# Kernel tuning notes

Measured on AMD Instinct MI355X. Metric: run time of the kernel, lower is better.

The kernel has to match this reference:

```python
import jax, jax.numpy as jnp
import numpy as np

N, E = 50000, 300000
IN, FC, AC, H, C1, C2, OUT = 1024, 128, 20, 4, 10, 5, 3
FCN = FC + AC + H * C2  # 168


def bn_eval(x, g, b):
    # BatchNorm1d in eval mode with running_mean=0, running_var=1
    return x * (g / jnp.sqrt(1.0 + 1e-5)) + b


def add_self_loops(edge_index, edge_attr, n):
    # PyG add_self_loops with fill_value='mean': self-loop attr = mean of incoming edge attrs
    src, dst = edge_index[0], edge_index[1]
    ones = jnp.ones(src.shape[0], jnp.float32)
    deg = jax.ops.segment_sum(ones, dst, num_segments=n)
    mean_attr = jax.ops.segment_sum(edge_attr, dst, num_segments=n) / jnp.maximum(deg, 1.0)[:, None]
    loop = jnp.arange(n, dtype=src.dtype)
    return (jnp.concatenate([src, loop]), jnp.concatenate([dst, loop]),
            jnp.concatenate([edge_attr, mean_attr], 0))


def gatv2(x, src, dst, eattr, Wl, bl, Wr, br, We, att, b, n):
    # GATv2Conv (concat=True, negative_slope=0.2, edge_dim=1)
    h, c = att.shape
    xl = (x @ Wl + bl).reshape(n, h, c)
    xr = (x @ Wr + br).reshape(n, h, c)
    em = (eattr @ We).reshape(-1, h, c)
    m = jax.nn.leaky_relu(xl[src] + xr[dst] + em, 0.2)   # [E', H, C]
    logit = jnp.einsum('ehc,hc->eh', m, att)              # [E', H]
    mx = jax.ops.segment_max(logit, dst, num_segments=n)
    ex = jnp.exp(logit - mx[dst])
    den = jax.ops.segment_sum(ex, dst, num_segments=n)
    alpha = ex / (den[dst] + 1e-16)                       # segment softmax over dst
    out = jax.ops.segment_sum(xl[src] * alpha[..., None], dst, num_segments=n)
    return out.reshape(n, h * c) + b


def setup_inputs() -> dict:
    key = jax.random.key(0)
    ks = jax.random.split(key, 24)
    rn = lambda k, s: jax.random.normal(k, s, jnp.float32) * 0.05
    return {
        'features': jax.random.normal(ks[0], (N, IN), jnp.float32),
        'edges': jax.random.randint(ks[1], (2, E), 0, N),
        'edges2': jax.random.randint(ks[2], (2, E), 0, N),
        'edge_features': jax.random.normal(ks[3], (E, 1), jnp.float32),
        'additional_features': jax.random.normal(ks[4], (N, AC), jnp.float32),
        'sage_Wl': rn(ks[5], (IN, FC)), 'sage_bl': jnp.zeros((FC,), jnp.float32),
        'sage_Wr': rn(ks[6], (IN, FC)),
        'g1_Wl': rn(ks[7], (AC, H * C1)), 'g1_bl': jnp.zeros((H * C1,), jnp.float32),
        'g1_Wr': rn(ks[8], (AC, H * C1)), 'g1_br': jnp.zeros((H * C1,), jnp.float32),
        'g1_We': rn(ks[9], (1, H * C1)), 'g1_att': rn(ks[10], (H, C1)),
        'g1_b': jnp.zeros((H * C1,), jnp.float32),
        'g2_Wl': rn(ks[11], (H * C1, H * C2)), 'g2_bl': jnp.zeros((H * C2,), jnp.float32),
        'g2_Wr': rn(ks[12], (H * C1, H * C2)), 'g2_br': jnp.zeros((H * C2,), jnp.float32),
        'g2_We': rn(ks[13], (1, H * C2)), 'g2_att': rn(ks[14], (H, C2)),
        'g2_b': jnp.zeros((H * C2,), jnp.float32),
        'fc1_W': rn(ks[15], (FCN, FCN)), 'fc1_b': jnp.zeros((FCN,), jnp.float32),
        'fc2_W': rn(ks[16], (FCN, OUT)), 'fc2_b': jnp.zeros((OUT,), jnp.float32),
        'bnx_g': jnp.ones((FC,), jnp.float32), 'bnx_b': jnp.zeros((FC,), jnp.float32),
        'bny_g': jnp.ones((H * C2,), jnp.float32), 'bny_b': jnp.zeros((H * C2,), jnp.float32),
        'bnf_g': jnp.ones((FCN,), jnp.float32), 'bnf_b': jnp.zeros((FCN,), jnp.float32),
    }


def reference(features, edges, edges2, edge_features, additional_features,
              sage_Wl, sage_bl, sage_Wr,
              g1_Wl, g1_bl, g1_Wr, g1_br, g1_We, g1_att, g1_b,
              g2_Wl, g2_bl, g2_Wr, g2_br, g2_We, g2_att, g2_b,
              fc1_W, fc1_b, fc2_W, fc2_b,
              bnx_g, bnx_b, bny_g, bny_b, bnf_g, bnf_b):
    n = features.shape[0]
    # --- SAGEConv (mean aggr): out = lin_l(mean_j x_j) + lin_r(x_i) ---
    src, dst = edges[0], edges[1]
    deg = jax.ops.segment_sum(jnp.ones(src.shape[0], jnp.float32), dst, num_segments=n)
    aggr = jax.ops.segment_sum(features[src], dst, num_segments=n) / jnp.maximum(deg, 1.0)[:, None]
    x = aggr @ sage_Wl + sage_bl + features @ sage_Wr
    x = bn_eval(x, bnx_g, bnx_b)
    # --- GATv2 stack (self loops with mean edge-attr fill) ---
    s2, d2, ea = add_self_loops(edges2, edge_features, n)
    y = gatv2(additional_features, s2, d2, ea, g1_Wl, g1_bl, g1_Wr, g1_br, g1_We, g1_att, g1_b, n)
    y = jax.nn.leaky_relu(y, 0.01)  # activation (dropout off in eval)
    y = gatv2(y, s2, d2, ea, g2_Wl, g2_bl, g2_Wr, g2_br, g2_We, g2_att, g2_b, n)
    y = bn_eval(y, bny_g, bny_b)
    # --- MLP head ---
    z = jax.nn.leaky_relu(jnp.concatenate([x, y], axis=1), 0.01)
    z = jnp.concatenate([z, additional_features], axis=1) @ fc1_W + fc1_b
    z = jax.nn.relu(bn_eval(z, bnf_g, bnf_b))
    return z @ fc2_W + fc2_b
```

## Files before the change

kernel.cpp:

```cpp
#include <hip/hip_runtime.h>
#include <hip/hip_bf16.h>
#include <cfloat>

__device__ __forceinline__ float lrelu(float x, float a) { return x > 0.0f ? x : a * x; }

__device__ __forceinline__ unsigned short f2bf(float f) {
    unsigned u = __float_as_uint(f);
    unsigned r = (u + 0x7FFFu + ((u >> 16) & 1u)) >> 16;
    return (unsigned short)r;
}
__device__ __forceinline__ float bf2f(unsigned short u) {
    return __uint_as_float((unsigned)u << 16);
}

typedef __attribute__((ext_vector_type(8))) short short8;
typedef __attribute__((ext_vector_type(4))) float f32x4;

#define BN_RSQ 0.99999500003749968750f
#define SCAN_B 256

__global__ void zero_ws(uint4* __restrict__ p, int n16)
{
    int t = blockIdx.x * blockDim.x + threadIdx.x;
    if (t < n16) p[t] = make_uint4(0u, 0u, 0u, 0u);
}

__global__ void prep_all(const float* __restrict__ sWl, const float* __restrict__ sWr,
                         unsigned short* __restrict__ Btp,
                         const float* __restrict__ fc1W, unsigned short* __restrict__ Bt1p,
                         const float* __restrict__ g1Wl, const float* __restrict__ g1Wr,
                         unsigned short* __restrict__ Bg1,
                         const float* __restrict__ g2Wl, const float* __restrict__ g2Wr,
                         unsigned short* __restrict__ Bg2,
                         const int* __restrict__ e1d, const int* __restrict__ e2d,
                         const float* __restrict__ ef,
                         int* __restrict__ cnt1, int* __restrict__ cnt2,
                         float* __restrict__ easum, float* __restrict__ eaext, int E)
{
    int idx = blockIdx.x * blockDim.x + threadIdx.x;
    if (idx < 262144) {
        int j = idx & 7, lane = (idx >> 3) & 63, fn = (idx >> 9) & 3, wid = (idx >> 11) & 3, t = idx >> 13;
        int c = wid * 64 + fn * 16 + (lane & 15);
        int k = t * 32 + (lane >> 4) * 8 + j;
        float v = (c < 128) ? sWl[(size_t)k * 128 + c] : sWr[(size_t)k * 128 + (c - 128)];
        Btp[idx] = f2bf(v);
        return;
    }
    idx -= 262144;
    if (idx < 36864) {
        int j = idx & 7, lane = (idx >> 3) & 63, fn = (idx >> 9) & 3, q = idx >> 11;
        int wid = q % 3, t = q / 3;
        int c = wid * 64 + fn * 16 + (lane & 15);
        int k = t * 32 + (lane >> 4) * 8 + j;
        float v = (c < 168 && k < 168) ? fc1W[(size_t)k * 168 + c] : 0.0f;
        Bt1p[idx] = f2bf(v);
        return;
    }
    idx -= 36864;
    if (idx < 2560) {
        int j = idx & 7, lane = (idx >> 3) & 63, fn = idx >> 9;
        int c = fn * 16 + (lane & 15);
        int k = (lane >> 4) * 8 + j;
        float v = 0.0f;
        if (k < 20) v = (c < 40) ? g1Wl[(size_t)k * 40 + c] : g1Wr[(size_t)k * 40 + (c - 40)];
        Bg1[idx] = f2bf(v);
        return;
    }
    idx -= 2560;
    if (idx < 3072) {
        int j = idx & 7, lane = (idx >> 3) & 63, q = idx >> 9;
        int fn = q % 3, t = q / 3;
        int c = fn * 16 + (lane & 15);
        int k = t * 32 + (lane >> 4) * 8 + j;
        float v = 0.0f;
        if (k < 40 && c < 40) v = (c < 20) ? g2Wl[(size_t)k * 20 + c] : g2Wr[(size_t)k * 20 + (c - 20)];
        Bg2[idx] = f2bf(v);
        return;
    }
    idx -= 3072;
    if (idx < E) {
        atomicAdd(&cnt1[e1d[idx]], 1);
        int d2 = e2d[idx];
        atomicAdd(&cnt2[d2], 1);
        float a = ef[idx];
        atomicAdd(&easum[d2], a);
        eaext[idx] = a;
    }
}

__global__ __launch_bounds__(256) void gemm_sage_mfma(
    const float* __restrict__ A, const unsigned short* __restrict__ Btp,
    unsigned short* __restrict__ P, int M)
{
    __shared__ unsigned short As2[2][64][72];
    const int tid = threadIdx.x;
    const int wid = tid >> 6, lane = tid & 63;
    const int m0 = blockIdx.x * 64;
    const int l16 = lane & 15, g = lane >> 4;
    const int colbase = wid * 64 + l16;
    const short8* Bv = reinterpret_cast<const short8*>(Btp);
    const int srow = tid >> 4, scol = (tid & 15) * 4;

    f32x4 acc[4][4] = {};
    float4 rcur[4], rnext[4];

#pragma unroll
    for (int p = 0; p < 4; ++p) {
        int ar = m0 + p * 16 + srow;
        rcur[p] = make_float4(0.f, 0.f, 0.f, 0.f);
        if (ar < M) rcur[p] = *reinterpret_cast<const float4*>(&A[(size_t)ar * 1024 + scol]);
    }
#pragma unroll
    for (int p = 0; p < 4; ++p) {
        ushort4 u;
        u.x = f2bf(rcur[p].x); u.y = f2bf(rcur[p].y); u.z = f2bf(rcur[p].z); u.w = f2bf(rcur[p].w);
        *reinterpret_cast<ushort4*>(&As2[0][p * 16 + srow][scol]) = u;
    }
#pragma unroll
    for (int p = 0; p < 4; ++p) {
        int ar = m0 + p * 16 + srow;
        rcur[p] = make_float4(0.f, 0.f, 0.f, 0.f);
        if (ar < M) rcur[p] = *reinterpret_cast<const float4*>(&A[(size_t)ar * 1024 + 64 + scol]);
    }
    __syncthreads();

    for (int c = 0; c < 16; ++c) {
        const int buf = c & 1;
        if (c < 14) {
            const int k0 = (c + 2) * 64;
#pragma unroll
            for (int p = 0; p < 4; ++p) {
                int ar = m0 + p * 16 + srow;
                rnext[p] = make_float4(0.f, 0.f, 0.f, 0.f);
                if (ar < M) rnext[p] = *reinterpret_cast<const float4*>(&A[(size_t)ar * 1024 + k0 + scol]);
            }
        }
#pragma unroll
        for (int t = 0; t < 2; ++t) {
            const int ks = c * 2 + t;
            short8 afr[4], bfr[4];
#pragma unroll
            for (int fm = 0; fm < 4; ++fm)
                afr[fm] = *reinterpret_cast<const short8*>(&As2[buf][fm * 16 + l16][t * 32 + g * 8]);
#pragma unroll
            for (int fn = 0; fn < 4; ++fn)
                bfr[fn] = Bv[((ks * 4 + wid) * 4 + fn) * 64 + lane];
#pragma unroll
            for (int fm = 0; fm < 4; ++fm)
#pragma unroll
                for (int fn = 0; fn < 4; ++fn)
                    acc[fm][fn] = __builtin_amdgcn_mfma_f32_16x16x32_bf16(
                        afr[fm], bfr[t == 0 ? fn : fn], acc[fm][fn], 0, 0, 0);
        }
        if (c < 15) {
#pragma unroll
            for (int p = 0; p < 4; ++p) {
                ushort4 u;
                u.x = f2bf(rcur[p].x); u.y = f2bf(rcur[p].y);
                u.z = f2bf(rcur[p].z); u.w = f2bf(rcur[p].w);
                *reinterpret_cast<ushort4*>(&As2[buf ^ 1][p * 16 + srow][scol]) = u;
            }
        }
        __syncthreads();
#pragma unroll
        for (int p = 0; p < 4; ++p) rcur[p] = rnext[p];
    }

#pragma unroll
    for (int fm = 0; fm < 4; ++fm) {
#pragma unroll
        for (int r = 0; r < 4; ++r) {
            int row = m0 + fm * 16 + g * 4 + r;
            if (row < M) {
#pragma unroll
                for (int fn = 0; fn < 4; ++fn)
                    P[(size_t)row * 256 + colbase + fn * 16] = f2bf(acc[fm][fn][r]);
            }
        }
    }
}

template <int IND, int KS, int NF, int MODE>
__global__ __launch_bounds__(64) void gat_lin_mfma(
    const float* __restrict__ X, const unsigned short* __restrict__ Bp,
    const float* __restrict__ bl, const float* __restrict__ br,
    float* __restrict__ xl, float* __restrict__ xr, int M)
{
    constexpr int W = KS * 32;
    constexpr int WP = W + 8;
    __shared__ unsigned short xs[64][WP];
    const int lane = threadIdx.x;
    const int m0 = blockIdx.x * 64;
    const int l16 = lane & 15, g = lane >> 4;
    const short8* Bv = reinterpret_cast<const short8*>(Bp);

    constexpr int NV = 64 * IND / 4 / 64;
#pragma unroll
    for (int i = 0; i < NV; ++i) {
        int q = i * 64 + lane;
        int f = q * 4;
        int row = f / IND, col = f % IND;
        int ar = m0 + row;
        float4 v = make_float4(0.f, 0.f, 0.f, 0.f);
        if (ar < M) v = *reinterpret_cast<const float4*>(&X[(size_t)ar * IND + col]);
        ushort4 u;
        u.x = f2bf(v.x); u.y = f2bf(v.y); u.z = f2bf(v.z); u.w = f2bf(v.w);
        *reinterpret_cast<ushort4*>(&xs[row][col]) = u;
    }
    ushort4 zz; zz.x = 0; zz.y = 0; zz.z = 0; zz.w = 0;
#pragma unroll
    for (int c = IND; c < W; c += 4)
        *reinterpret_cast<ushort4*>(&xs[lane][c]) = zz;

    f32x4 acc[4][NF] = {};
#pragma unroll
    for (int t = 0; t < KS; ++t) {
        short8 afr[4], bfr[NF];
#pragma unroll
        for (int fm = 0; fm < 4; ++fm)
            afr[fm] = *reinterpret_cast<const short8*>(&xs[fm * 16 + l16][t * 32 + g * 8]);
#pragma unroll
        for (int fn = 0; fn < NF; ++fn)
            bfr[fn] = Bv[(t * NF + fn) * 64 + lane];
#pragma unroll
        for (int fm = 0; fm < 4; ++fm)
#pragma unroll
            for (int fn = 0; fn < NF; ++fn)
                acc[fm][fn] = __builtin_amdgcn_mfma_f32_16x16x32_bf16(
                    afr[fm], bfr[fn], acc[fm][fn], 0, 0, 0);
    }

#pragma unroll
    for (int fm = 0; fm < 4; ++fm) {
#pragma unroll
        for (int r = 0; r < 4; ++r) {
            int row = m0 + fm * 16 + g * 4 + r;
            if (row < M) {
#pragma unroll
                for (int fn = 0; fn < NF; ++fn) {
                    int col = fn * 16 + l16;
                    float v = acc[fm][fn][r];
                    if (MODE == 1) {
                        if (col < 40) xl[(size_t)row * 40 + col] = v + bl[col];
                        else          xr[(size_t)row * 40 + (col - 40)] = v + br[col - 40];
                    } else {
                        if (col < 20)      xl[(size_t)row * 20 + col] = v + bl[col];
                        else if (col < 40) xr[(size_t)row * 20 + (col - 20)] = v + br[col - 20];
                    }
                }
            }
        }
    }
}

__global__ __launch_bounds__(256) void mlp_mfma(
    const unsigned short* __restrict__ z, const float* __restrict__ addf,
    const unsigned short* __restrict__ Bt1p,
    const float* __restrict__ fc1b, const float* __restrict__ bnfg, const float* __restrict__ bnfb,
    const float* __restrict__ fc2W, const float* __restrict__ fc2b,
    float* __restrict__ out, int M)
{
    __shared__ __align__(16) char smem[64 * 169 * 4];
    unsigned short (*zs)[200] = reinterpret_cast<unsigned short(*)[200]>(smem);
    float (*ts)[169] = reinterpret_cast<float(*)[169]>(smem);
    const int tid = threadIdx.x;
    const int wid = tid >> 6, lane = tid & 63;
    const int m0 = blockIdx.x * 64;
    const int l16 = lane & 15, g = lane >> 4;
    const short8* Bv = reinterpret_cast<const short8*>(Bt1p);

#pragma unroll
    for (int p = 0; p < 13; ++p) {
        int idx = p * 256 + tid;
        if (idx < 3200) {
            int row = idx / 50, c4 = (idx % 50) * 4;
            int ar = m0 + row;
            ushort4 u; u.x = 0; u.y = 0; u.z = 0; u.w = 0;
            if (ar < M) {
                if (c4 < 148) {
                    u = *reinterpret_cast<const ushort4*>(&z[(size_t)ar * 168 + c4]);
                } else if (c4 < 168) {
                    float4 v = *reinterpret_cast<const float4*>(&addf[(size_t)ar * 20 + (c4 - 148)]);
                    u.x = f2bf(v.x); u.y = f2bf(v.y); u.z = f2bf(v.z); u.w = f2bf(v.w);
                }
            }
            *reinterpret_cast<ushort4*>(&zs[row][c4]) = u;
        }
    }
    __syncthreads();

    f32x4 acc[4][4] = {};
    if (wid < 3) {
#pragma unroll
        for (int t = 0; t < 6; ++t) {
            short8 afr[4], bfr[4];
#pragma unroll
            for (int fm = 0; fm < 4; ++fm)
                afr[fm] = *reinterpret_cast<const short8*>(&zs[fm * 16 + l16][t * 32 + g * 8]);
#pragma unroll
            for (int fn = 0; fn < 4; ++fn)
                bfr[fn] = Bv[((t * 3 + wid) * 4 + fn) * 64 + lane];
#pragma unroll
            for (int fm = 0; fm < 4; ++fm)
#pragma unroll
                for (int fn = 0; fn < 4; ++fn)
                    acc[fm][fn] = __builtin_amdgcn_mfma_f32_16x16x32_bf16(
                        afr[fm], bfr[fn], acc[fm][fn], 0, 0, 0);
        }
    }
    __syncthreads();
    if (wid < 3) {
        const int colbase = wid * 64 + l16;
#pragma unroll
        for (int fm = 0; fm < 4; ++fm) {
#pragma unroll
            for (int r = 0; r < 4; ++r) {
                int rr = fm * 16 + g * 4 + r;
#pragma unroll
                for (int fn = 0; fn < 4; ++fn) {
                    int col = colbase + fn * 16;
                    if (col < 168) {
                        float v = acc[fm][fn][r] + fc1b[col];
                        v = v * (bnfg[col] * BN_RSQ) + bnfb[col];
                        ts[rr][col] = fmaxf(v, 0.0f);
                    }
                }
            }
        }
    }
    __syncthreads();
    if (tid < 192) {
        int r = tid & 63, c = tid >> 6;
        float acc2 = fc2b[c];
#pragma unroll 4
        for (int k = 0; k < 168; ++k) acc2 += ts[r][k] * fc2W[k * 3 + c];
        int row = m0 + r;
        if (row < M) out[(size_t)row * 3 + c] = acc2;
    }
}

__global__ void scan1(const int* __restrict__ cnt1, const int* __restrict__ cnt2,
                      int* __restrict__ off1, int* __restrict__ off2,
                      int* __restrict__ bsum1, int* __restrict__ bsum2, int M)
{
    __shared__ int sh[SCAN_B];
    int y = blockIdx.y;
    const int* cnt = y ? cnt2 : cnt1;
    int* excl = y ? off2 : off1;
    int* bsum = y ? bsum2 : bsum1;
    int i = blockIdx.x * SCAN_B + threadIdx.x;
    int v = (i < M) ? cnt[i] + y : 0;
    sh[threadIdx.x] = v;
    __syncthreads();
    for (int o = 1; o < SCAN_B; o <<= 1) {
        int t = (threadIdx.x >= o) ? sh[threadIdx.x - o] : 0;
        __syncthreads();
        sh[threadIdx.x] += t;
        __syncthreads();
    }
    if (i < M) excl[i] = sh[threadIdx.x] - v;
    if (threadIdx.x == SCAN_B - 1) bsum[blockIdx.x] = sh[threadIdx.x];
}

__global__ void scan2(int* __restrict__ bsum1, int* __restrict__ bsum2, int nb)
{
    __shared__ int sh[SCAN_B];
    int* bsum = blockIdx.y ? bsum2 : bsum1;
    int v = ((int)threadIdx.x < nb) ? bsum[threadIdx.x] : 0;
    sh[threadIdx.x] = v;
    __syncthreads();
    for (int o = 1; o < SCAN_B; o <<= 1) {
        int t = (threadIdx.x >= o) ? sh[threadIdx.x - o] : 0;
        __syncthreads();
        sh[threadIdx.x] += t;
        __syncthreads();
    }
    if ((int)threadIdx.x < nb) bsum[threadIdx.x] = sh[threadIdx.x] - v;
}

__global__ void scan3(int* __restrict__ off1, int* __restrict__ off2,
                      const int* __restrict__ bsum1, const int* __restrict__ bsum2,
                      const int* __restrict__ cnt1, const int* __restrict__ cnt2,
                      const float* __restrict__ easum, float* __restrict__ eaext,
                      int E, int M)
{
    int y = blockIdx.y;
    int* off = y ? off2 : off1;
    const int* bsum = y ? bsum2 : bsum1;
    const int* cnt = y ? cnt2 : cnt1;
    int i = blockIdx.x * SCAN_B + threadIdx.x;
    if (i < M) {
        int v = off[i] + bsum[blockIdx.x];
        off[i] = v;
        if (i == M - 1) off[M] = v + cnt[i] + y;
        if (y) eaext[E + i] = easum[i] / fmaxf((float)cnt2[i], 1.0f);
    }
}

__global__ void fill_both(const int* __restrict__ e1s, const int* __restrict__ e1d,
                          const int* __restrict__ e2d,
                          const int* __restrict__ off1, const int* __restrict__ off2,
                          int* __restrict__ cnt1, int* __restrict__ cnt2,
                          int* __restrict__ srcs1, int* __restrict__ eidx2, int E, int Eext)
{
    int t = blockIdx.x * blockDim.x + threadIdx.x;
    if (t < E) {
        int d = e1d[t];
        int pos = atomicSub(&cnt1[d], 1) - 1;
        srcs1[off1[d] + pos] = e1s[t];
    }
    int t2 = t - E;
    if (t2 >= 0 && t2 < Eext) {
        if (t2 < E) {
            int d = e2d[t2];
            int pos = atomicSub(&cnt2[d], 1) - 1;
            eidx2[off2[d] + pos] = t2;
        } else {
            int nn = t2 - E;
            eidx2[off2[nn + 1] - 1] = t2;
        }
    }
}

__global__ void sage_gather(const int* __restrict__ srcs1, const int* __restrict__ off1,
                            const unsigned short* __restrict__ P, const float* __restrict__ bl,
                            const float* __restrict__ bng, const float* __restrict__ bnb,
                            unsigned short* __restrict__ z, int N)
{
    int t = blockIdx.x * blockDim.x + threadIdx.x;
    if (t >= N * 32) return;
    int n = t >> 5, g = t & 31;
    int beg = off1[n], end = off1[n + 1];
    float a0 = 0.f, a1 = 0.f, a2 = 0.f, a3 = 0.f;
    for (int j = beg; j < end; ++j) {
        int s = srcs1[j];
        ushort4 v = *reinterpret_cast<const ushort4*>(&P[(size_t)s * 256 + g * 4]);
        a0 += bf2f(v.x); a1 += bf2f(v.y); a2 += bf2f(v.z); a3 += bf2f(v.w);
    }
    float inv = 1.0f / fmaxf((float)(end - beg), 1.0f);
    ushort4 pr = *reinterpret_cast<const ushort4*>(&P[(size_t)n * 256 + 128 + g * 4]);
    float a4[4] = {a0, a1, a2, a3};
    float p4[4] = {bf2f(pr.x), bf2f(pr.y), bf2f(pr.z), bf2f(pr.w)};
    ushort4 zo;
    unsigned short* zp = reinterpret_cast<unsigned short*>(&zo);
#pragma unroll
    for (int k = 0; k < 4; ++k) {
        int cc = g * 4 + k;
        float x = a4[k] * inv + bl[cc] + p4[k];
        x = x * (bng[cc] * BN_RSQ) + bnb[cc];
        zp[k] = f2bf(lrelu(x, 0.01f));
    }
    *reinterpret_cast<ushort4*>(&z[(size_t)n * 168 + g * 4]) = zo;
}

template <int H, int C, int MODE>
__global__ void gat_node(const int* __restrict__ eidx2, const int* __restrict__ off2,
                         const int* __restrict__ e2s, const float* __restrict__ eaext,
                         const float* __restrict__ xl, const float* __restrict__ xr,
                         const float* __restrict__ We, const float* __restrict__ att,
                         const float* __restrict__ b,
                         const float* __restrict__ bng, const float* __restrict__ bnb,
                         void* __restrict__ outv, int E, int N)
{
    int t = blockIdx.x * blockDim.x + threadIdx.x;
    if (t >= N * H) return;
    int n = t / H, h = t % H;

    float xrc[C], atth[C], weh[C];
#pragma unroll
    for (int c = 0; c < C; ++c) {
        xrc[c]  = xr[(size_t)n * (H * C) + h * C + c];
        atth[c] = att[h * C + c];
        weh[c]  = We[h * C + c];
    }

    const int beg = off2[n], end = off2[n + 1];

    float mx = -FLT_MAX, den = 0.0f;
    float accv[C] = {};
    for (int j = beg; j < end; ++j) {
        int e = eidx2[j];
        int s = (e < E) ? e2s[e] : (e - E);
        float ea = eaext[e];
        const float* xls = xl + (size_t)s * (H * C) + h * C;
        float xv[C];
        float lg = 0.0f;
#pragma unroll
        for (int c = 0; c < C; ++c) {
            xv[c] = xls[c];
            float m = xv[c] + xrc[c] + ea * weh[c];
            lg += lrelu(m, 0.2f) * atth[c];
        }
        if (lg > mx) {
            float sc = __expf(mx - lg);
            den *= sc;
#pragma unroll
            for (int c = 0; c < C; ++c) accv[c] *= sc;
            mx = lg;
        }
        float ex = __expf(lg - mx);
        den += ex;
#pragma unroll
        for (int c = 0; c < C; ++c) accv[c] += ex * xv[c];
    }
    float inv = 1.0f / (den + 1e-16f);

#pragma unroll
    for (int c = 0; c < C; ++c) {
        int jch = h * C + c;
        float v = accv[c] * inv + b[jch];
        if (MODE == 1) {
            ((float*)outv)[(size_t)n * (H * C) + jch] = lrelu(v, 0.01f);
        } else {
            v = v * (bng[jch] * BN_RSQ) + bnb[jch];
            ((unsigned short*)outv)[(size_t)n * 168 + 128 + jch] = f2bf(lrelu(v, 0.01f));
        }
    }
}

extern "C" void kernel_launch(void* const* d_in, const int* in_sizes, int n_in,
                              void* d_out, int out_size, void* d_ws, size_t ws_size,
                              hipStream_t stream)
{
    const float* features = (const float*)d_in[0];
    const int*   e1       = (const int*)d_in[1];
    const int*   e2       = (const int*)d_in[2];
    const float* ef       = (const float*)d_in[3];
    const float* addf     = (const float*)d_in[4];
    const float* sage_Wl  = (const float*)d_in[5];
    const float* sage_bl  = (const float*)d_in[6];
    const float* sage_Wr  = (const float*)d_in[7];
    const float* g1_Wl = (const float*)d_in[8];
    const float* g1_bl = (const float*)d_in[9];
    const float* g1_Wr = (const float*)d_in[10];
    const float* g1_br = (const float*)d_in[11];
    const float* g1_We = (const float*)d_in[12];
    const float* g1_att = (const float*)d_in[13];
    const float* g1_b = (const float*)d_in[14];
    const float* g2_Wl = (const float*)d_in[15];
    const float* g2_bl = (const float*)d_in[16];
    const float* g2_Wr = (const float*)d_in[17];
    const float* g2_br = (const float*)d_in[18];
    const float* g2_We = (const float*)d_in[19];
    const float* g2_att = (const float*)d_in[20];
    const float* g2_b = (const float*)d_in[21];
    const float* fc1_W = (const float*)d_in[22];
    const float* fc1_b = (const float*)d_in[23];
    const float* fc2_W = (const float*)d_in[24];
    const float* fc2_b = (const float*)d_in[25];
    const float* bnx_g = (const float*)d_in[26];
    const float* bnx_b = (const float*)d_in[27];
    const float* bny_g = (const float*)d_in[28];
    const float* bny_b = (const float*)d_in[29];
    const float* bnf_g = (const float*)d_in[30];
    const float* bnf_b = (const float*)d_in[31];

    const int N = in_sizes[0] / 1024;
    const int E = in_sizes[3];
    const int Eext = E + N;
    const int* e1s = e1, *e1d = e1 + E;
    const int* e2s = e2, *e2d = e2 + E;
    const int nb = (N + SCAN_B - 1) / SCAN_B;

    char* wb = (char*)d_ws;
    size_t off = 0;
    auto takeB = [&](size_t bytes) { char* p = wb + off; off = (off + bytes + 255) & ~(size_t)255; return p; };
    unsigned short* P = (unsigned short*)takeB((size_t)N * 256 * 2);
    unsigned short* z = (unsigned short*)takeB((size_t)N * 168 * 2);
    float* eaext = (float*)takeB((size_t)Eext * 4);
    float* xl1   = (float*)takeB((size_t)N * 40 * 4);
    float* xr1   = (float*)takeB((size_t)N * 40 * 4);
    float* y1    = (float*)takeB((size_t)N * 40 * 4);
    float* xl2   = (float*)takeB((size_t)N * 20 * 4);
    float* xr2   = (float*)takeB((size_t)N * 20 * 4);
    unsigned short* Btp  = (unsigned short*)takeB((size_t)256 * 1024 * 2);
    unsigned short* Bt1p = (unsigned short*)takeB((size_t)36864 * 2);
    unsigned short* Bg1  = (unsigned short*)takeB((size_t)2560 * 2);
    unsigned short* Bg2  = (unsigned short*)takeB((size_t)3072 * 2);
    char* zero_beg = wb + off;
    int* cnt1    = (int*)takeB((size_t)N * 4);
    int* cnt2    = (int*)takeB((size_t)N * 4);
    float* easum = (float*)takeB((size_t)N * 4);
    size_t zero_len = (size_t)((wb + off) - zero_beg);
    int* off1  = (int*)takeB((size_t)(N + 1) * 4);
    int* off2  = (int*)takeB((size_t)(N + 1) * 4);
    int* bsum1 = (int*)takeB(SCAN_B * 4);
    int* bsum2 = (int*)takeB(SCAN_B * 4);
    int* srcs1 = (int*)takeB((size_t)E * 4);
    int* eidx2 = (int*)takeB((size_t)Eext * 4);

    const int B = 256;
    const int n16 = (int)(zero_len / 16);
    zero_ws<<<(n16 + B - 1) / B, B, 0, stream>>>((uint4*)zero_beg, n16);

    const int prep_total = 262144 + 36864 + 2560 + 3072 + E;
    prep_all<<<(prep_total + B - 1) / B, B, 0, stream>>>(
        sage_Wl, sage_Wr, Btp, fc1_W, Bt1p,
        g1_Wl, g1_Wr, Bg1, g2_Wl, g2_Wr, Bg2,
        e1d, e2d, ef, cnt1, cnt2, easum, eaext, E);

    scan1<<<dim3(nb, 2), SCAN_B, 0, stream>>>(cnt1, cnt2, off1, off2, bsum1, bsum2, N);
    scan2<<<dim3(1, 2), SCAN_B, 0, stream>>>(bsum1, bsum2, nb);
    scan3<<<dim3(nb, 2), SCAN_B, 0, stream>>>(off1, off2, bsum1, bsum2, cnt1, cnt2,
                                              easum, eaext, E, N);

    fill_both<<<(E + Eext + B - 1) / B, B, 0, stream>>>(e1s, e1d, e2d, off1, off2,
                                                        cnt1, cnt2, srcs1, eidx2, E, Eext);

    const int mtiles = (N + 63) / 64;
    gemm_sage_mfma<<<mtiles, 256, 0, stream>>>(features, Btp, P, N);
    sage_gather<<<(N * 32 + B - 1) / B, B, 0, stream>>>(srcs1, off1, P, sage_bl, bnx_g, bnx_b, z, N);

    gat_lin_mfma<20, 1, 5, 1><<<mtiles, 64, 0, stream>>>(addf, Bg1, g1_bl, g1_br, xl1, xr1, N);
    gat_node<4, 10, 1><<<(N * 4 + B - 1) / B, B, 0, stream>>>(
        eidx2, off2, e2s, eaext, xl1, xr1, g1_We, g1_att, g1_b,
        nullptr, nullptr, (void*)y1, E, N);

    gat_lin_mfma<40, 2, 3, 2><<<mtiles, 64, 0, stream>>>(y1, Bg2, g2_bl, g2_br, xl2, xr2, N);
    gat_node<4, 5, 2><<<(N * 4 + B - 1) / B, B, 0, stream>>>(
        eidx2, off2, e2s, eaext, xl2, xr2, g2_We, g2_att, g2_b,
        bny_g, bny_b, (void*)z, E, N);

    mlp_mfma<<<mtiles, 256, 0, stream>>>(z, addf, Bt1p, fc1_b, bnf_g, bnf_b, fc2_W, fc2_b,
                                         (float*)d_out, N);
}
```

Measured before the change: 292.6 us.

## Stage SAGE GEMM A tiles via direct global-to-LDS loads with XOR swizzle

The SAGE projection GEMM now copies fp32 A tiles straight into shared memory with global_load_lds, instead of loading them into registers, converting to bf16 and writing to LDS. Tiles are stored in fp32 with an XOR-swizzled column layout to avoid bank conflicts, and the bf16 conversion moves to fragment-read time. This is meant to free registers and VALU work from the staging path and to overlap loads asynchronously. In exchange it doubles the LDS footprint, repeats the conversion per fragment read, and cuts prefetch depth from two tiles to one.

```diff
diff --git a/kernel.cpp b/kernel.cpp
--- a/kernel.cpp
+++ b/kernel.cpp
@@ -92,56 +92,64 @@
     const float* __restrict__ A, const unsigned short* __restrict__ Btp,
     unsigned short* __restrict__ P, int M)
 {
-    __shared__ unsigned short As2[2][64][72];
+    __shared__ float As2[2][64][64];
     const int tid = threadIdx.x;
     const int wid = tid >> 6, lane = tid & 63;
     const int m0 = blockIdx.x * 64;
     const int l16 = lane & 15, g = lane >> 4;
     const int colbase = wid * 64 + l16;
     const short8* Bv = reinterpret_cast<const short8*>(Btp);
-    const int srow = tid >> 4, scol = (tid & 15) * 4;
+    const int r4 = lane >> 4;
+    const int cgp = lane & 15;
+
+    int srow[4]; const float* sga[4];
+#pragma unroll
+    for (int i = 0; i < 4; ++i) {
+        int row = wid * 16 + i * 4 + r4;
+        int cgl = cgp ^ (row & 7);
+        int ar = m0 + row; if (ar >= M) ar = M - 1;
+        srow[i] = row;
+        sga[i] = &A[(size_t)ar * 1024 + cgl * 4];
+    }
+
+    auto stage = [&](int buf, int k0f) {
+#pragma unroll
+        for (int i = 0; i < 4; ++i) {
+            const float* gp = sga[i] + k0f;
+            float* lp = &As2[buf][wid * 16 + i * 4][0];
+            __builtin_amdgcn_global_load_lds(
+                (const __attribute__((address_space(1))) void*)gp,
+                (__attribute__((address_space(3))) void*)lp, 16, 0, 0);
+        }
+    };
 
     f32x4 acc[4][4] = {};
-    float4 rcur[4], rnext[4];
-
-#pragma unroll
-    for (int p = 0; p < 4; ++p) {
-        int ar = m0 + p * 16 + srow;
-        rcur[p] = make_float4(0.f, 0.f, 0.f, 0.f);
-        if (ar < M) rcur[p] = *reinterpret_cast<const float4*>(&A[(size_t)ar * 1024 + scol]);
-    }
-#pragma unroll
-    for (int p = 0; p < 4; ++p) {
-        ushort4 u;
-        u.x = f2bf(rcur[p].x); u.y = f2bf(rcur[p].y); u.z = f2bf(rcur[p].z); u.w = f2bf(rcur[p].w);
-        *reinterpret_cast<ushort4*>(&As2[0][p * 16 + srow][scol]) = u;
-    }
-#pragma unroll
-    for (int p = 0; p < 4; ++p) {
-        int ar = m0 + p * 16 + srow;
-        rcur[p] = make_float4(0.f, 0.f, 0.f, 0.f);
-        if (ar < M) rcur[p] = *reinterpret_cast<const float4*>(&A[(size_t)ar * 1024 + 64 + scol]);
-    }
+
+    stage(0, 0);
     __syncthreads();
 
     for (int c = 0; c < 16; ++c) {
         const int buf = c & 1;
-        if (c < 14) {
-            const int k0 = (c + 2) * 64;
-#pragma unroll
-            for (int p = 0; p < 4; ++p) {
-                int ar = m0 + p * 16 + srow;
-                rnext[p] = make_float4(0.f, 0.f, 0.f, 0.f);
-                if (ar < M) rnext[p] = *reinterpret_cast<const float4*>(&A[(size_t)ar * 1024 + k0 + scol]);
-            }
-        }
+        if (c < 15) stage(buf ^ 1, (c + 1) * 64);
 #pragma unroll
         for (int t = 0; t < 2; ++t) {
             const int ks = c * 2 + t;
             short8 afr[4], bfr[4];
 #pragma unroll
-            for (int fm = 0; fm < 4; ++fm)
-                afr[fm] = *reinterpret_cast<const short8*>(&As2[buf][fm * 16 + l16][t * 32 + g * 8]);
+            for (int fm = 0; fm < 4; ++fm) {
+                int row = fm * 16 + l16;
+                int cg0 = t * 8 + g * 2;
+                int p0 = cg0 ^ (row & 7);
+                int p1 = (cg0 + 1) ^ (row & 7);
+                f32x4 lo = *reinterpret_cast<const f32x4*>(&As2[buf][row][p0 * 4]);
+                f32x4 hi = *reinterpret_cast<const f32x4*>(&As2[buf][row][p1 * 4]);
+                short8 a;
+                a[0] = (short)f2bf(lo[0]); a[1] = (short)f2bf(lo[1]);
+                a[2] = (short)f2bf(lo[2]); a[3] = (short)f2bf(lo[3]);
+                a[4] = (short)f2bf(hi[0]); a[5] = (short)f2bf(hi[1]);
+                a[6] = (short)f2bf(hi[2]); a[7] = (short)f2bf(hi[3]);
+                afr[fm] = a;
+            }
 #pragma unroll
             for (int fn = 0; fn < 4; ++fn)
                 bfr[fn] = Bv[((ks * 4 + wid) * 4 + fn) * 64 + lane];
@@ -150,20 +158,9 @@
 #pragma unroll
                 for (int fn = 0; fn < 4; ++fn)
                     acc[fm][fn] = __builtin_amdgcn_mfma_f32_16x16x32_bf16(
-                        afr[fm], bfr[t == 0 ? fn : fn], acc[fm][fn], 0, 0, 0);
-        }
-        if (c < 15) {
-#pragma unroll
-            for (int p = 0; p < 4; ++p) {
-                ushort4 u;
-                u.x = f2bf(rcur[p].x); u.y = f2bf(rcur[p].y);
-                u.z = f2bf(rcur[p].z); u.w = f2bf(rcur[p].w);
-                *reinterpret_cast<ushort4*>(&As2[buf ^ 1][p * 16 + srow][scol]) = u;
-            }
+                        afr[fm], bfr[fn], acc[fm][fn], 0, 0, 0);
         }
         __syncthreads();
-#pragma unroll
-        for (int p = 0; p < 4; ++p) rcur[p] = rnext[p];
     }
 
 #pragma unroll
```

Result: slower. 302.9 us (+3.5%).

## Pack GAT edge source and attribute into CSR and pad per-head features

Applied to the files above, without the earlier changes.

The dst-sorted GAT edge list now stores (source, edge-attribute) pairs directly, so the gather no longer goes edge-id → e2s → eaext through extra indirect loads. The GAT linear outputs are written in a per-head layout padded to 12 or 8 floats, so the node kernels can read each head with float4 loads. The SAGE gather moves to 16 threads per node with 8-wide bf16 loads. In exchange, the padded buffers are larger and the pad slots are never written, so uninitialised workspace values feed into the padded arithmetic.

```diff
diff --git a/kernel.cpp b/kernel.cpp
--- a/kernel.cpp
+++ b/kernel.cpp
@@ -35,7 +35,7 @@
                          const int* __restrict__ e1d, const int* __restrict__ e2d,
                          const float* __restrict__ ef,
                          int* __restrict__ cnt1, int* __restrict__ cnt2,
-                         float* __restrict__ easum, float* __restrict__ eaext, int E)
+                         float* __restrict__ easum, int E)
 {
     int idx = blockIdx.x * blockDim.x + threadIdx.x;
     if (idx < 262144) {
@@ -82,9 +82,7 @@
         atomicAdd(&cnt1[e1d[idx]], 1);
         int d2 = e2d[idx];
         atomicAdd(&cnt2[d2], 1);
-        float a = ef[idx];
-        atomicAdd(&easum[d2], a);
-        eaext[idx] = a;
+        atomicAdd(&easum[d2], ef[idx]);
     }
 }
 
@@ -150,7 +148,7 @@
 #pragma unroll
                 for (int fn = 0; fn < 4; ++fn)
                     acc[fm][fn] = __builtin_amdgcn_mfma_f32_16x16x32_bf16(
-                        afr[fm], bfr[t == 0 ? fn : fn], acc[fm][fn], 0, 0, 0);
+                        afr[fm], bfr[fn], acc[fm][fn], 0, 0, 0);
         }
         if (c < 15) {
 #pragma unroll
@@ -241,11 +239,21 @@
                     int col = fn * 16 + l16;
                     float v = acc[fm][fn][r];
                     if (MODE == 1) {
-                        if (col < 40) xl[(size_t)row * 40 + col] = v + bl[col];
-                        else          xr[(size_t)row * 40 + (col - 40)] = v + br[col - 40];
+                        if (col < 40) {
+                            int h = col / 10, c = col % 10;
+                            xl[((size_t)row * 4 + h) * 12 + c] = v + bl[col];
+                        } else if (col < 80) {
+                            int cc = col - 40, h = cc / 10, c = cc % 10;
+                            xr[((size_t)row * 4 + h) * 12 + c] = v + br[cc];
+                        }
                     } else {
-                        if (col < 20)      xl[(size_t)row * 20 + col] = v + bl[col];
-                        else if (col < 40) xr[(size_t)row * 20 + (col - 20)] = v + br[col - 20];
+                        if (col < 20) {
+                            int h = col / 5, c = col % 5;
+                            xl[((size_t)row * 4 + h) * 8 + c] = v + bl[col];
+                        } else if (col < 40) {
+                            int cc = col - 20, h = cc / 5, c = cc % 5;
+                            xr[((size_t)row * 4 + h) * 8 + c] = v + br[cc];
+                        }
                     }
                 }
             }
@@ -381,8 +389,7 @@
 __global__ void scan3(int* __restrict__ off1, int* __restrict__ off2,
                       const int* __restrict__ bsum1, const int* __restrict__ bsum2,
                       const int* __restrict__ cnt1, const int* __restrict__ cnt2,
-                      const float* __restrict__ easum, float* __restrict__ eaext,
-                      int E, int M)
+                      const float* __restrict__ easum, float* __restrict__ ealoop, int M)
 {
     int y = blockIdx.y;
     int* off = y ? off2 : off1;
@@ -393,15 +400,16 @@
         int v = off[i] + bsum[blockIdx.x];
         off[i] = v;
         if (i == M - 1) off[M] = v + cnt[i] + y;
-        if (y) eaext[E + i] = easum[i] / fmaxf((float)cnt2[i], 1.0f);
+        if (y) ealoop[i] = easum[i] / fmaxf((float)cnt2[i], 1.0f);
     }
 }
 
 __global__ void fill_both(const int* __restrict__ e1s, const int* __restrict__ e1d,
-                          const int* __restrict__ e2d,
+                          const int* __restrict__ e2s, const int* __restrict__ e2d,
+                          const float* __restrict__ ef, const float* __restrict__ ealoop,
                           const int* __restrict__ off1, const int* __restrict__ off2,
                           int* __restrict__ cnt1, int* __restrict__ cnt2,
-                          int* __restrict__ srcs1, int* __restrict__ eidx2, int E, int Eext)
+                          int* __restrict__ srcs1, int2* __restrict__ se2, int E, int Eext)
 {
     int t = blockIdx.x * blockDim.x + threadIdx.x;
     if (t < E) {
@@ -414,10 +422,10 @@
         if (t2 < E) {
             int d = e2d[t2];
             int pos = atomicSub(&cnt2[d], 1) - 1;
-            eidx2[off2[d] + pos] = t2;
+            se2[off2[d] + pos] = make_int2(e2s[t2], __float_as_int(ef[t2]));
         } else {
             int nn = t2 - E;
-            eidx2[off2[nn + 1] - 1] = t2;
+            se2[off2[nn + 1] - 1] = make_int2(nn, __float_as_int(ealoop[nn]));
         }
     }
 }
@@ -428,66 +436,72 @@
                             unsigned short* __restrict__ z, int N)
 {
     int t = blockIdx.x * blockDim.x + threadIdx.x;
-    if (t >= N * 32) return;
-    int n = t >> 5, g = t & 31;
+    if (t >= N * 16) return;
+    int n = t >> 4, g = t & 15;
     int beg = off1[n], end = off1[n + 1];
-    float a0 = 0.f, a1 = 0.f, a2 = 0.f, a3 = 0.f;
+    float a[8] = {};
     for (int j = beg; j < end; ++j) {
         int s = srcs1[j];
-        ushort4 v = *reinterpret_cast<const ushort4*>(&P[(size_t)s * 256 + g * 4]);
-        a0 += bf2f(v.x); a1 += bf2f(v.y); a2 += bf2f(v.z); a3 += bf2f(v.w);
+        short8 v = *reinterpret_cast<const short8*>(&P[(size_t)s * 256 + g * 8]);
+#pragma unroll
+        for (int k = 0; k < 8; ++k) a[k] += bf2f((unsigned short)v[k]);
     }
     float inv = 1.0f / fmaxf((float)(end - beg), 1.0f);
-    ushort4 pr = *reinterpret_cast<const ushort4*>(&P[(size_t)n * 256 + 128 + g * 4]);
-    float a4[4] = {a0, a1, a2, a3};
-    float p4[4] = {bf2f(pr.x), bf2f(pr.y), bf2f(pr.z), bf2f(pr.w)};
-    ushort4 zo;
-    unsigned short* zp = reinterpret_cast<unsigned short*>(&zo);
-#pragma unroll
-    for (int k = 0; k < 4; ++k) {
-        int cc = g * 4 + k;
-        float x = a4[k] * inv + bl[cc] + p4[k];
+    short8 pr = *reinterpret_cast<const short8*>(&P[(size_t)n * 256 + 128 + g * 8]);
+    short8 zo;
+#pragma unroll
+    for (int k = 0; k < 8; ++k) {
+        int cc = g * 8 + k;
+        float x = a[k] * inv + bl[cc] + bf2f((unsigned short)pr[k]);
         x = x * (bng[cc] * BN_RSQ) + bnb[cc];
-        zp[k] = f2bf(lrelu(x, 0.01f));
-    }
-    *reinterpret_cast<ushort4*>(&z[(size_t)n * 168 + g * 4]) = zo;
-}
-
-template <int H, int C, int MODE>
-__global__ void gat_node(const int* __restrict__ eidx2, const int* __restrict__ off2,
-                         const int* __restrict__ e2s, const float* __restrict__ eaext,
+        zo[k] = (short)f2bf(lrelu(x, 0.01f));
+    }
+    *reinterpret_cast<short8*>(&z[(size_t)n * 168 + g * 8]) = zo;
+}
+
+template <int H, int C, int PAD, int MODE>
+__global__ void gat_node(const int2* __restrict__ se2, const int* __restrict__ off2,
                          const float* __restrict__ xl, const float* __restrict__ xr,
                          const float* __restrict__ We, const float* __restrict__ att,
                          const float* __restrict__ b,
                          const float* __restrict__ bng, const float* __restrict__ bnb,
-                         void* __restrict__ outv, int E, int N)
+                         void* __restrict__ outv, int N)
 {
     int t = blockIdx.x * blockDim.x + threadIdx.x;
     if (t >= N * H) return;
     int n = t / H, h = t % H;
 
-    float xrc[C], atth[C], weh[C];
-#pragma unroll
-    for (int c = 0; c < C; ++c) {
-        xrc[c]  = xr[(size_t)n * (H * C) + h * C + c];
-        atth[c] = att[h * C + c];
-        weh[c]  = We[h * C + c];
+    float xrc[PAD], atth[PAD], weh[PAD];
+    const float4* xrp = reinterpret_cast<const float4*>(&xr[((size_t)n * H + h) * PAD]);
+#pragma unroll
+    for (int q = 0; q < PAD / 4; ++q) {
+        float4 v = xrp[q];
+        xrc[q * 4 + 0] = v.x; xrc[q * 4 + 1] = v.y; xrc[q * 4 + 2] = v.z; xrc[q * 4 + 3] = v.w;
+    }
+#pragma unroll
+    for (int c = 0; c < PAD; ++c) {
+        atth[c] = (c < C) ? att[h * C + c] : 0.0f;
+        weh[c]  = (c < C) ? We[h * C + c]  : 0.0f;
     }
 
     const int beg = off2[n], end = off2[n + 1];
 
     float mx = -FLT_MAX, den = 0.0f;
-    float accv[C] = {};
+    float accv[PAD] = {};
     for (int j = beg; j < end; ++j) {
-        int e = eidx2[j];
-        int s = (e < E) ? e2s[e] : (e - E);
-        float ea = eaext[e];
-        const float* xls = xl + (size_t)s * (H * C) + h * C;
-        float xv[C];
+        int2 se = se2[j];
+        int s = se.x;
+        float ea = __int_as_float(se.y);
+        const float4* xlp = reinterpret_cast<const float4*>(&xl[((size_t)s * H + h) * PAD]);
+        float xv[PAD];
+#pragma unroll
+        for (int q = 0; q < PAD / 4; ++q) {
+            float4 v = xlp[q];
+            xv[q * 4 + 0] = v.x; xv[q * 4 + 1] = v.y; xv[q * 4 + 2] = v.z; xv[q * 4 + 3] = v.w;
+        }
         float lg = 0.0f;
 #pragma unroll
-        for (int c = 0; c < C; ++c) {
-            xv[c] = xls[c];
+        for (int c = 0; c < PAD; ++c) {
             float m = xv[c] + xrc[c] + ea * weh[c];
             lg += lrelu(m, 0.2f) * atth[c];
         }
@@ -495,13 +509,13 @@
             float sc = __expf(mx - lg);
             den *= sc;
 #pragma unroll
-            for (int c = 0; c < C; ++c) accv[c] *= sc;
+            for (int c = 0; c < PAD; ++c) accv[c] *= sc;
             mx = lg;
         }
         float ex = __expf(lg - mx);
         den += ex;
 #pragma unroll
-        for (int c = 0; c < C; ++c) accv[c] += ex * xv[c];
+        for (int c = 0; c < PAD; ++c) accv[c] += ex * xv[c];
     }
     float inv = 1.0f / (den + 1e-16f);
 
@@ -567,12 +581,12 @@
     auto takeB = [&](size_t bytes) { char* p = wb + off; off = (off + bytes + 255) & ~(size_t)255; return p; };
     unsigned short* P = (unsigned short*)takeB((size_t)N * 256 * 2);
     unsigned short* z = (unsigned short*)takeB((size_t)N * 168 * 2);
-    float* eaext = (float*)takeB((size_t)Eext * 4);
-    float* xl1   = (float*)takeB((size_t)N * 40 * 4);
-    float* xr1   = (float*)takeB((size_t)N * 40 * 4);
+    float* ealoop = (float*)takeB((size_t)N * 4);
+    float* xl1   = (float*)takeB((size_t)N * 48 * 4);
+    float* xr1   = (float*)takeB((size_t)N * 48 * 4);
     float* y1    = (float*)takeB((size_t)N * 40 * 4);
-    float* xl2   = (float*)takeB((size_t)N * 20 * 4);
-    float* xr2   = (float*)takeB((size_t)N * 20 * 4);
+    float* xl2   = (float*)takeB((size_t)N * 32 * 4);
+    float* xr2   = (float*)takeB((size_t)N * 32 * 4);
     unsigned short* Btp  = (unsigned short*)takeB((size_t)256 * 1024 * 2);
     unsigned short* Bt1p = (unsigned short*)takeB((size_t)36864 * 2);
     unsigned short* Bg1  = (unsigned short*)takeB((size_t)2560 * 2);
@@ -587,7 +601,7 @@
     int* bsum1 = (int*)takeB(SCAN_B * 4);
     int* bsum2 = (int*)takeB(SCAN_B * 4);
     int* srcs1 = (int*)takeB((size_t)E * 4);
-    int* eidx2 = (int*)takeB((size_t)Eext * 4);
+    int2* se2  = (int2*)takeB((size_t)Eext * 8);
 
     const int B = 256;
     const int n16 = (int)(zero_len / 16);
@@ -597,29 +611,28 @@
     prep_all<<<(prep_total + B - 1) / B, B, 0, stream>>>(
         sage_Wl, sage_Wr, Btp, fc1_W, Bt1p,
         g1_Wl, g1_Wr, Bg1, g2_Wl, g2_Wr, Bg2,
-        e1d, e2d, ef, cnt1, cnt2, easum, eaext, E);
+        e1d, e2d, ef, cnt1, cnt2, easum, E);
 
     scan1<<<dim3(nb, 2), SCAN_B, 0, stream>>>(cnt1, cnt2, off1, off2, bsum1, bsum2, N);
     scan2<<<dim3(1, 2), SCAN_B, 0, stream>>>(bsum1, bsum2, nb);
     scan3<<<dim3(nb, 2), SCAN_B, 0, stream>>>(off1, off2, bsum1, bsum2, cnt1, cnt2,
-                                              easum, eaext, E, N);
-
-    fill_both<<<(E + Eext + B - 1) / B, B, 0, stream>>>(e1s, e1d, e2d, off1, off2,
-                                                        cnt1, cnt2, srcs1, eidx2, E, Eext);
+                                              easum, ealoop, N);
+
+    fill_both<<<(E + Eext + B - 1) / B, B, 0, stream>>>(e1s, e1d, e2s, e2d, ef, ealoop,
+                                                        off1, off2, cnt1, cnt2,
+                                                        srcs1, se2, E, Eext);
 
     const int mtiles = (N + 63) / 64;
     gemm_sage_mfma<<<mtiles, 256, 0, stream>>>(features, Btp, P, N);
-    sage_gather<<<(N * 32 + B - 1) / B, B, 0, stream>>>(srcs1, off1, P, sage_bl, bnx_g, bnx_b, z, N);
+    sage_gather<<<(N * 16 + B - 1) / B, B, 0, stream>>>(srcs1, off1, P, sage_bl, bnx_g, bnx_b, z, N);
 
     gat_lin_mfma<20, 1, 5, 1><<<mtiles, 64, 0, stream>>>(addf, Bg1, g1_bl, g1_br, xl1, xr1, N);
-    gat_node<4, 10, 1><<<(N * 4 + B - 1) / B, B, 0, stream>>>(
-        eidx2, off2, e2s, eaext, xl1, xr1, g1_We, g1_att, g1_b,
-        nullptr, nullptr, (void*)y1, E, N);
+    gat_node<4, 10, 12, 1><<<(N * 4 + B - 1) / B, B, 0, stream>>>(
+        se2, off2, xl1, xr1, g1_We, g1_att, g1_b, nullptr, nullptr, (void*)y1, N);
 
     gat_lin_mfma<40, 2, 3, 2><<<mtiles, 64, 0, stream>>>(y1, Bg2, g2_bl, g2_br, xl2, xr2, N);
-    gat_node<4, 5, 2><<<(N * 4 + B - 1) / B, B, 0, stream>>>(
-        eidx2, off2, e2s, eaext, xl2, xr2, g2_We, g2_att, g2_b,
-        bny_g, bny_b, (void*)z, E, N);
+    gat_node<4, 5, 8, 2><<<(N * 4 + B - 1) / B, B, 0, stream>>>(
+        se2, off2, xl2, xr2, g2_We, g2_att, g2_b, bny_g, bny_b, (void*)z, N);
 
     mlp_mfma<<<mtiles, 256, 0, stream>>>(z, addf, Bt1p, fc1_b, bnf_g, bnf_b, fc2_W, fc2_b,
                                          (float*)d_out, N);
```

Measured after the change: 296.8 us. No clear change (+1.4%).
